# Kernel tuning notes

Measured on AMD Instinct MI355X. Metric: run time of the kernel, lower is better.

The kernel has to match this reference:

```python
import jax, jax.numpy as jnp
import numpy as np
import math

# ---- static config (matches init_kwargs) ----
LMAX = 2; NC = (LMAX + 1) ** 2        # 9 spherical components
H = 8; DQK = 32; CV = 16; K = 8       # heads, qk dim, value head dim, radial freqs
NTH = 5; NPH = 5; U = NTH * NPH       # 25 sphere directions
N = 2048; C = 256

# ---- Clebsch-Gordan in the real spherical-harmonic basis (numpy, tiny) ----
def _cg(j1, m1, j2, m2, j, m):
    if m1 + m2 != m or j < abs(j1 - j2) or j > j1 + j2:
        return 0.0
    f = math.factorial
    pref = math.sqrt((2 * j + 1) * f(j + j1 - j2) * f(j - j1 + j2) * f(j1 + j2 - j) / f(j1 + j2 + j + 1))
    pref *= math.sqrt(f(j + m) * f(j - m) * f(j1 - m1) * f(j1 + m1) * f(j2 - m2) * f(j2 + m2))
    s = 0.0
    for k in range(0, j1 + j2 - j + 1):
        d = [k, j1 + j2 - j - k, j1 - m1 - k, j2 + m2 - k, j - j2 + m1 + k, j - j1 - m2 + k]
        if min(d) < 0:
            continue
        s += (-1) ** k / (f(d[0]) * f(d[1]) * f(d[2]) * f(d[3]) * f(d[4]) * f(d[5]))
    return pref * s

def _Umat(l):
    u = np.zeros((2 * l + 1, 2 * l + 1), dtype=np.complex128)
    s = 1.0 / math.sqrt(2.0)
    for m in range(-l, l + 1):
        if m > 0:
            u[l + m, l + m] = ((-1) ** m) * s; u[l + m, l - m] = s
        elif m == 0:
            u[l, l] = 1.0
        else:
            u[l + m, l + m] = 1j * s; u[l + m, l - m] = -1j * ((-1) ** m) * s
    return u

def _real_cg(l1, l2, L):
    cgc = np.zeros((2 * l1 + 1, 2 * l2 + 1, 2 * L + 1))
    for i1, m1 in enumerate(range(-l1, l1 + 1)):
        for i2, m2 in enumerate(range(-l2, l2 + 1)):
            for i3, m3 in enumerate(range(-L, L + 1)):
                cgc[i1, i2, i3] = _cg(l1, m1, l2, m2, L, m3)
    r = np.einsum('au,bv,cw,uvw->abc', _Umat(l1), _Umat(l2), np.conj(_Umat(L)), cgc)
    re, im = np.real(r), np.imag(r)
    return re if np.linalg.norm(re) >= np.linalg.norm(im) else im

def _right_reduced():
    off = [0, 1, 4]
    R = np.zeros((NC, NC, NC)); cnt = np.zeros(LMAX + 1)
    for l1 in range(LMAX + 1):
        for l2 in range(LMAX + 1):
            for L in range(abs(l1 - l2), min(l1 + l2, LMAX) + 1):
                R[off[l1]:off[l1] + 2 * l1 + 1, off[l2]:off[l2] + 2 * l2 + 1, off[L]:off[L] + 2 * L + 1] += _real_cg(l1, l2, L)
                cnt[L] += 1
    for L in range(LMAX + 1):
        R[:, :, off[L]:off[L] + 2 * L + 1] /= max(cnt[L], 1.0)
    return R

def _sphere():
    x, w = np.polynomial.legendre.leggauss(NTH)
    phi = 2 * np.pi * np.arange(NPH) / NPH
    ct = np.repeat(x, NPH); wq = np.repeat(w, NPH) * (2 * np.pi / NPH)
    ph = np.tile(phi, NTH); st = np.sqrt(np.maximum(1 - ct * ct, 0.0))
    dirs = np.stack([st * np.cos(ph), st * np.sin(ph), ct], axis=1)
    return dirs, wq

def _ymat(d):
    x, y, z = d[:, 0], d[:, 1], d[:, 2]
    return np.stack([0.282095 * np.ones_like(x), 0.488603 * y, 0.488603 * z, 0.488603 * x,
                     1.092548 * x * y, 1.092548 * y * z, 0.315392 * (3 * z * z - 1),
                     1.092548 * x * z, 0.546274 * (x * x - y * y)], axis=0)  # [9,U]

_DIRS, _WQ = _sphere()
_YW = _ymat(_DIRS) * _WQ[None, :]          # quadrature-weighted Y_l(u): [9,U]
_RRED = _right_reduced()                    # CG coupling ell x lambda -> L<=lmax: [9,9,9]
_LDEG = np.array([0, 1, 1, 1, 2, 2, 2, 2, 2])


def setup_inputs() -> dict:
    key = jax.random.key(0)
    ks = jax.random.split(key, 8)
    node_pos = 3.0 * jax.random.normal(ks[0], (N, 3), dtype=jnp.float32)
    node_feat = jax.random.normal(ks[1], (N, NC, C), dtype=jnp.float32)
    Wq = 0.02 * jax.random.normal(ks[2], (3, C, H * DQK), dtype=jnp.float32)
    Wk = 0.02 * jax.random.normal(ks[3], (3, C, H * DQK), dtype=jnp.float32)
    Wv = jax.random.normal(ks[4], (C, H * CV), dtype=jnp.float32) / math.sqrt(C)
    Wo = jax.random.normal(ks[5], (H * CV, C), dtype=jnp.float32) / math.sqrt(H * CV)
    kappa = jnp.linspace(1.0, 1.4, K, dtype=jnp.float32)
    bias = jnp.exp(-2.0 * (kappa - 1.0) / 0.4)          # low-kappa preference at init
    a = 0.05 * jax.random.normal(ks[6], (3, H, K), dtype=jnp.float32) * bias
    return {"node_pos": node_pos, "node_feat": node_feat, "Wq": Wq, "Wk": Wk,
            "Wv": Wv, "Wo": Wo, "a": a, "kappa": kappa}


def reference(node_pos, node_feat, Wq, Wk, Wv, Wo, a, kappa):
    YW = jnp.asarray(_YW, jnp.float32)
    RRED = jnp.asarray(_RRED, jnp.float32)
    DIRS = jnp.asarray(_DIRS, jnp.float32)
    aE = a[jnp.asarray(_LDEG)]                           # [9,H,K] radial coeffs per ell component

    def so3_to_scalar(x, W):  # invariant q/k projection from irreps
        s = x[:, 0, :] @ W[0]
        s = s + jnp.sqrt(jnp.sum(x[:, 1:4, :] ** 2, axis=1) + 1e-8) @ W[1]
        s = s + jnp.sqrt(jnp.sum(x[:, 4:9, :] ** 2, axis=1) + 1e-8) @ W[2]
        return s

    q = so3_to_scalar(node_feat, Wq).reshape(-1, H, DQK)
    k = so3_to_scalar(node_feat, Wk).reshape(-1, H, DQK)
    qf = jax.nn.elu(q) + 1.0                             # linear-attention feature map
    kf = jax.nn.elu(k) + 1.0
    # value irreps per head: [N,H,Cv,lambda=9]
    v = jnp.einsum('nmc,cf->nmf', node_feat, Wv).reshape(-1, NC, H, CV).transpose(0, 2, 3, 1)

    phase = kappa[None, :, None] * (node_pos @ DIRS.T)[:, None, :]   # [N,K,U]
    cosP = jnp.cos(phase); sinP = jnp.sin(phase)

    acc = jnp.zeros((node_pos.shape[0], H, CV, NC, NC), jnp.float32)  # [N,H,Cv,lambda,ell]
    for kk in range(K):  # small fixed radial-frequency loop
        ck = cosP[:, kk]; sk = sinP[:, kk]
        Yak = jnp.einsum('eu,eh->euh', YW, aE[:, :, kk])              # a_{l,h,k} * w_u * Y_e(u)
        # moments over all nodes (keys x values x phase): [U,H,d,Cv,lambda]
        Mc = jnp.einsum('nhd,nhcl,nu->uhdcl', kf, v, ck)
        Ms = jnp.einsum('nhd,nhcl,nu->uhdcl', kf, v, sk)
        Dc = jnp.einsum('nu,euh->neuh', ck, Yak)
        Ds = jnp.einsum('nu,euh->neuh', sk, Yak)
        acc = acc + jnp.einsum('nhd,uhdcl,neuh->nhcle', qf, Mc, Dc) \
                  + jnp.einsum('nhd,uhdcl,neuh->nhcle', qf, Ms, Ds)
    Z = jnp.einsum('nhd,hd->nh', qf, kf.sum(0)) + 1e-6               # linear-attn normalizer
    acc = acc / Z[:, :, None, None, None]
    # CG coupling ell (x) lambda -> L<=lmax, path-averaged: [N,H,Cv,9]
    outm = jnp.einsum('nhcle,elm->nhcm', acc, RRED)
    out = outm.transpose(0, 3, 1, 2).reshape(-1, NC, H * CV) @ Wo    # [N,9,C]
    return out
```

## Files before the change

### kernel.cpp

```cpp
#include <hip/hip_runtime.h>
#include <cmath>
#include <complex>
#include <algorithm>


typedef _Float16 half8 __attribute__((ext_vector_type(8)));
typedef _Float16 half4v __attribute__((ext_vector_type(4)));
typedef float float4v __attribute__((ext_vector_type(4)));

namespace {

using cd = std::complex<double>;

static double fct(int n) { double r = 1.0; for (int i = 2; i <= n; ++i) r *= i; return r; }

static double cg_coef(int j1, int m1, int j2, int m2, int j, int m) {
    if (m1 + m2 != m || j < std::abs(j1 - j2) || j > j1 + j2) return 0.0;
    double pref = std::sqrt((2 * j + 1) * fct(j + j1 - j2) * fct(j - j1 + j2) * fct(j1 + j2 - j) / fct(j1 + j2 + j + 1));
    pref *= std::sqrt(fct(j + m) * fct(j - m) * fct(j1 - m1) * fct(j1 + m1) * fct(j2 - m2) * fct(j2 + m2));
    double s = 0.0;
    for (int k = 0; k <= j1 + j2 - j; ++k) {
        int d0 = k, d1 = j1 + j2 - j - k, d2 = j1 - m1 - k, d3 = j2 + m2 - k, d4 = j - j2 + m1 + k, d5 = j - j1 - m2 + k;
        if (d0 < 0 || d1 < 0 || d2 < 0 || d3 < 0 || d4 < 0 || d5 < 0) continue;
        s += ((k & 1) ? -1.0 : 1.0) / (fct(d0) * fct(d1) * fct(d2) * fct(d3) * fct(d4) * fct(d5));
    }
    return pref * s;
}

static void umat(int l, cd u[5][5]) {
    for (int i = 0; i < 5; i++) for (int j = 0; j < 5; j++) u[i][j] = cd(0, 0);
    const double s = 1.0 / std::sqrt(2.0);
    for (int m = -l; m <= l; m++) {
        double sgn = (std::abs(m) & 1) ? -1.0 : 1.0;
        if (m > 0)      { u[l + m][l + m] = cd(sgn * s, 0); u[l + m][l - m] = cd(s, 0); }
        else if (m == 0){ u[l][l] = cd(1, 0); }
        else            { u[l + m][l + m] = cd(0, s);       u[l + m][l - m] = cd(0, -sgn * s); }
    }
}

static void real_cg_f(int l1, int l2, int L, double out[5][5][5]) {
    cd U1[5][5], U2[5][5], UL[5][5];
    umat(l1, U1); umat(l2, U2); umat(L, UL);
    const int n1 = 2 * l1 + 1, n2 = 2 * l2 + 1, n3 = 2 * L + 1;
    double cgt[5][5][5];
    for (int i1 = 0; i1 < n1; i1++) for (int i2 = 0; i2 < n2; i2++) for (int i3 = 0; i3 < n3; i3++)
        cgt[i1][i2][i3] = cg_coef(l1, i1 - l1, l2, i2 - l2, L, i3 - L);
    cd r[5][5][5];
    double nr = 0, ni = 0;
    for (int a1 = 0; a1 < n1; a1++) for (int b = 0; b < n2; b++) for (int c = 0; c < n3; c++) {
        cd acc(0, 0);
        for (int uu = 0; uu < n1; uu++) for (int vv = 0; vv < n2; vv++) for (int w = 0; w < n3; w++) {
            double cval = cgt[uu][vv][w];
            if (cval == 0.0) continue;
            acc += U1[a1][uu] * U2[b][vv] * std::conj(UL[c][w]) * cval;
        }
        r[a1][b][c] = acc;
        nr += acc.real() * acc.real();
        ni += acc.imag() * acc.imag();
    }
    const bool useRe = std::sqrt(nr) >= std::sqrt(ni);
    for (int a1 = 0; a1 < n1; a1++) for (int b = 0; b < n2; b++) for (int c = 0; c < n3; c++)
        out[a1][b][c] = useRe ? r[a1][b][c].real() : r[a1][b][c].imag();
}

static float  h_const[1029];
static float* d_const_g = nullptr;

struct GlobalInit {
    GlobalInit() {
        const double PI = 3.14159265358979323846;
        const double gx[5] = {-0.9061798459386640, -0.5384693101056831, 0.0, 0.5384693101056831, 0.9061798459386640};
        const double gw[5] = { 0.23692688505618908, 0.47862867049936647, 0.5688888888888889, 0.47862867049936647, 0.23692688505618908};
        double YW[9][25], DIRS[25][3];
        for (int u = 0; u < 25; ++u) {
            const int it = u / 5, ip = u % 5;
            const double ct = gx[it], wq = gw[it] * (2.0 * PI / 5.0), ph = 2.0 * PI * ip / 5.0;
            const double st = std::sqrt(std::max(1.0 - ct * ct, 0.0));
            const double x = st * std::cos(ph), y = st * std::sin(ph), z = ct;
            DIRS[u][0] = x; DIRS[u][1] = y; DIRS[u][2] = z;
            double Y[9];
            Y[0] = 0.282095;           Y[1] = 0.488603 * y;      Y[2] = 0.488603 * z;
            Y[3] = 0.488603 * x;       Y[4] = 1.092548 * x * y;  Y[5] = 1.092548 * y * z;
            Y[6] = 0.315392 * (3 * z * z - 1); Y[7] = 1.092548 * x * z; Y[8] = 0.546274 * (x * x - y * y);
            for (int e = 0; e < 9; e++) YW[e][u] = Y[e] * wq;
        }
        double RRED[9][9][9];
        for (int i = 0; i < 9; i++) for (int j = 0; j < 9; j++) for (int k = 0; k < 9; k++) RRED[i][j][k] = 0.0;
        const int off[3] = {0, 1, 4};
        double cnt[3] = {0, 0, 0};
        double rc[5][5][5];
        for (int l1 = 0; l1 <= 2; l1++) for (int l2 = 0; l2 <= 2; l2++) {
            const int Llo = std::abs(l1 - l2), Lhi = std::min(l1 + l2, 2);
            for (int L = Llo; L <= Lhi; L++) {
                real_cg_f(l1, l2, L, rc);
                for (int i1 = 0; i1 < 2 * l1 + 1; i1++)
                    for (int i2 = 0; i2 < 2 * l2 + 1; i2++)
                        for (int i3 = 0; i3 < 2 * L + 1; i3++)
                            RRED[off[l1] + i1][off[l2] + i2][off[L] + i3] += rc[i1][i2][i3];
                cnt[L] += 1.0;
            }
        }
        for (int L = 0; L <= 2; L++) {
            const double dv = std::max(cnt[L], 1.0);
            for (int a1 = 0; a1 < 9; a1++) for (int b = 0; b < 9; b++)
                for (int k = 0; k < 2 * L + 1; k++) RRED[a1][b][off[L] + k] /= dv;
        }
        for (int e = 0; e < 9; e++) for (int u = 0; u < 25; u++) h_const[e * 25 + u] = (float)YW[e][u];
        for (int e = 0; e < 9; e++) for (int l = 0; l < 9; l++) for (int m = 0; m < 9; m++)
            h_const[225 + e * 81 + l * 9 + m] = (float)RRED[e][l][m];
        for (int u = 0; u < 25; u++) for (int ax = 0; ax < 3; ax++) h_const[954 + u * 3 + ax] = (float)DIRS[u][ax];
        if (hipMalloc((void**)&d_const_g, 1029 * sizeof(float)) == hipSuccess)
            hipMemcpy(d_const_g, h_const, 1029 * sizeof(float), hipMemcpyHostToDevice);
    }
} g_init;

}


__global__ void radial_k(const float* __restrict__ feat, float* __restrict__ R) {
    const int n = blockIdx.x, c = threadIdx.x;
    const float* f = feat + (size_t)n * 9 * 256 + c;
    const float f0 = f[0];
    const float a1 = f[256], a2 = f[512], a3 = f[768];
    const float b1 = f[1024], b2 = f[1280], b3 = f[1536], b4 = f[1792], b5 = f[2048];
    const float r1 = sqrtf(a1 * a1 + a2 * a2 + a3 * a3 + 1e-8f);
    const float r2 = sqrtf(b1 * b1 + b2 * b2 + b3 * b3 + b4 * b4 + b5 * b5 + 1e-8f);
    float* o = R + (size_t)n * 768 + c;
    o[0] = f0; o[256] = r1; o[512] = r2;
}

__global__ __launch_bounds__(256) void qk_gemm_k(const float* __restrict__ A,
                                                 const float* __restrict__ Wq,
                                                 const float* __restrict__ Wk,
                                                 float* __restrict__ qf,
                                                 _Float16* __restrict__ kfA) {
    __shared__ __align__(16) _Float16 Af[64 * 40];
    __shared__ __align__(16) _Float16 Bf[64 * 40];
    const int tid = threadIdx.x;
    const int w = tid >> 6, lane = tid & 63;
    const int l15 = lane & 15, quad = lane >> 4;
    const bool isK = blockIdx.x >= 4;
    const int cb = (blockIdx.x & 3) * 64;
    const int rb = blockIdx.y * 64;
    const float* B = isK ? Wk : Wq;
    const int N = 256, Kd = 768;
    const int sr = tid >> 2, sq = tid & 3;

    float4v acc[4];
#pragma unroll
    for (int s = 0; s < 4; s++) acc[s] = float4v{0.f, 0.f, 0.f, 0.f};

    for (int k0 = 0; k0 < Kd; k0 += 32) {
        __syncthreads();
        {
            const float* Ap = A + (size_t)(rb + sr) * Kd + k0 + sq * 8;
            const float4 a0 = *(const float4*)(Ap);
            const float4 a1 = *(const float4*)(Ap + 4);
            half8 hv;
            hv[0] = (_Float16)a0.x; hv[1] = (_Float16)a0.y; hv[2] = (_Float16)a0.z; hv[3] = (_Float16)a0.w;
            hv[4] = (_Float16)a1.x; hv[5] = (_Float16)a1.y; hv[6] = (_Float16)a1.z; hv[7] = (_Float16)a1.w;
            *(half8*)&Af[sr * 40 + sq * 8] = hv;
        }
        {
            const float* Bp = B + (size_t)(k0 + sq * 8) * N + cb + sr;
            half8 hv;
#pragma unroll
            for (int i = 0; i < 8; i++) hv[i] = (_Float16)Bp[(size_t)i * N];
            *(half8*)&Bf[sr * 40 + sq * 8] = hv;
        }
        __syncthreads();
        const half8 af = *(const half8*)&Af[(w * 16 + l15) * 40 + quad * 8];
#pragma unroll
        for (int s = 0; s < 4; s++) {
            const half8 bf = *(const half8*)&Bf[(s * 16 + l15) * 40 + quad * 8];
            acc[s] = __builtin_amdgcn_mfma_f32_16x16x32_f16(af, bf, acc[s], 0, 0, 0);
        }
    }
#pragma unroll
    for (int s = 0; s < 4; s++) {
#pragma unroll
        for (int r = 0; r < 4; r++) {
            const int row = rb + w * 16 + quad * 4 + r;
            const int col = cb + s * 16 + l15;
            float val = acc[s][r];
            val = (val > 0.f ? val : expf(val) - 1.f) + 1.f;
            if (isK) {
                const int hh = col >> 5, dd = col & 31, tt = dd >> 4, ll = dd & 15;
                kfA[(size_t)hh * 65536 + (size_t)(row >> 5) * 1024 + tt * 512 + ll * 32 + (row & 31)] = (_Float16)val;
            } else {
                qf[(size_t)row * 256 + col] = val;
            }
        }
    }
}

__global__ __launch_bounds__(256) void mfma_gemm16_k(const float* __restrict__ A, const float* __restrict__ B,
                                                     float* __restrict__ Cv, int M, int N, int Kd, int mode,
                                                     const float* __restrict__ rZ) {
    __shared__ __align__(16) _Float16 Af[64 * 40];
    __shared__ __align__(16) _Float16 Bf[64 * 40];
    const int tid = threadIdx.x;
    const int w = tid >> 6, lane = tid & 63;
    const int l15 = lane & 15, quad = lane >> 4;
    const int rb = blockIdx.y * 64, cb = blockIdx.x * 64;
    const int sr = tid >> 2, sq = tid & 3;

    float4v acc[4];
#pragma unroll
    for (int s = 0; s < 4; s++) acc[s] = float4v{0.f, 0.f, 0.f, 0.f};

    for (int k0 = 0; k0 < Kd; k0 += 32) {
        __syncthreads();
        if (mode == 4) {
            const _Float16* Ap16 = (const _Float16*)A + (size_t)(rb + sr) * Kd + k0 + sq * 8;
            const half8 p0 = *(const half8*)(Ap16);
            const half8 p1 = *(const half8*)(Ap16 + 2359296);
            const half8 p2 = *(const half8*)(Ap16 + 4718592);
            const half8 p3 = *(const half8*)(Ap16 + 7077888);
            const int n = (rb + sr) / 9;
            const int hh = (k0 + sq * 8) >> 4;
            const float rz = rZ[n * 8 + hh];
            half8 hv;
#pragma unroll
            for (int i = 0; i < 8; i++)
                hv[i] = (_Float16)(((float)p0[i] + (float)p1[i] + (float)p2[i] + (float)p3[i]) * rz);
            *(half8*)&Af[sr * 40 + sq * 8] = hv;
        } else {
            const float* Ap = A + (size_t)(rb + sr) * Kd + k0 + sq * 8;
            const float4 a0 = *(const float4*)(Ap);
            const float4 a1 = *(const float4*)(Ap + 4);
            half8 hv;
            hv[0] = (_Float16)a0.x; hv[1] = (_Float16)a0.y; hv[2] = (_Float16)a0.z; hv[3] = (_Float16)a0.w;
            hv[4] = (_Float16)a1.x; hv[5] = (_Float16)a1.y; hv[6] = (_Float16)a1.z; hv[7] = (_Float16)a1.w;
            *(half8*)&Af[sr * 40 + sq * 8] = hv;
        }
        {
            const float* Bp = B + (size_t)(k0 + sq * 8) * N + cb + sr;
            half8 hv;
#pragma unroll
            for (int i = 0; i < 8; i++) hv[i] = (_Float16)Bp[(size_t)i * N];
            *(half8*)&Bf[sr * 40 + sq * 8] = hv;
        }
        __syncthreads();
        const half8 af = *(const half8*)&Af[(w * 16 + l15) * 40 + quad * 8];
#pragma unroll
        for (int s = 0; s < 4; s++) {
            const half8 bf = *(const half8*)&Bf[(s * 16 + l15) * 40 + quad * 8];
            acc[s] = __builtin_amdgcn_mfma_f32_16x16x32_f16(af, bf, acc[s], 0, 0, 0);
        }
    }
#pragma unroll
    for (int s = 0; s < 4; s++) {
#pragma unroll
        for (int r = 0; r < 4; r++) {
            const int row = rb + w * 16 + quad * 4 + r;
            const int col = cb + s * 16 + l15;
            float val = acc[s][r];
            if (mode == 2) {
                const int n = row / 9, l = row - n * 9, hq = col >> 4, cvq = col & 15;
                _Float16* o = (_Float16*)Cv;
                o[((size_t)hq * 144 + cvq * 9 + l) * 2048 + n] = (_Float16)val;
            } else {
                Cv[(size_t)row * N + col] = val;
            }
        }
    }
}

__global__ void trig_k(const float* __restrict__ pos, const float* __restrict__ kappa,
                       const float* __restrict__ cst, _Float16* __restrict__ trigA) {
    const int n = blockIdx.x, t = threadIdx.x;
    const size_t base = (size_t)(n >> 5) * 16384 + (n & 31);
    if (t < 200) {
        const int kq = t / 25, u = t - kq * 25;
        const float* dirs = cst + 954;
        const float ph = kappa[kq] * (pos[n * 3] * dirs[u * 3] + pos[n * 3 + 1] * dirs[u * 3 + 1] + pos[n * 3 + 2] * dirs[u * 3 + 2]);
        float s, c;
        sincosf(ph, &s, &c);
        const int kkut = (kq * 25 + u) * 2;
        trigA[base + (size_t)kkut * 32] = (_Float16)c;
        trigA[base + (size_t)(kkut + 1) * 32] = (_Float16)s;
    } else {
        const int kkut = 400 + (t - 200) * 2;
        trigA[base + (size_t)kkut * 32] = (_Float16)0.f;
        trigA[base + (size_t)(kkut + 1) * 32] = (_Float16)0.f;
    }
}

__global__ void ksumT_k(const _Float16* __restrict__ kfA, float* __restrict__ ksum) {
    const int b = blockIdx.x;
    const int h = b >> 5, d = b & 31, t = d >> 4, l15 = d & 15;
    const int i = threadIdx.x;
    const half8 v = *(const half8*)(kfA + (size_t)h * 65536 + (size_t)(i >> 2) * 1024 + t * 512 + l15 * 32 + (i & 3) * 8);
    float s = 0.f;
#pragma unroll
    for (int k = 0; k < 8; k++) s += (float)v[k];
#pragma unroll
    for (int off = 32; off > 0; off >>= 1) s += __shfl_down(s, off, 64);
    __shared__ float red[4];
    if ((i & 63) == 0) red[i >> 6] = s;
    __syncthreads();
    if (i == 0) ksum[b] = red[0] + red[1] + red[2] + red[3];
}

__global__ void zg_k(const float* __restrict__ qf, const float* __restrict__ ksum, float* __restrict__ rz,
                     const float* __restrict__ a, const float* __restrict__ cst, float* __restrict__ G) {
    if (blockIdx.x < 64) {
        const int idx = blockIdx.x * 256 + threadIdx.x;
        const int n = idx >> 3, h = idx & 7;
        float s = 0.f;
#pragma unroll
        for (int d = 0; d < 32; d++) s += qf[(size_t)n * 256 + h * 32 + d] * ksum[h * 32 + d];
        rz[idx] = 1.0f / (s + 1e-6f);
    } else {
        const int b = blockIdx.x - 64;
        const int kk = b & 7, h = b >> 3;
        __shared__ float ae[9];
        if (threadIdx.x < 9) {
            const int ldeg[9] = {0, 1, 1, 1, 2, 2, 2, 2, 2};
            ae[threadIdx.x] = a[ldeg[threadIdx.x] * 64 + h * 8 + kk];
        }
        __syncthreads();
        const float* yw = cst;
        const float* rred = cst + 225;
        for (int i = threadIdx.x; i < 25 * 81; i += 256) {
            const int u = i / 81, lm = i - u * 81;
            float s = 0.f;
#pragma unroll
            for (int e = 0; e < 9; e++) s += ae[e] * yw[e * 25 + u] * rred[e * 81 + lm];
            G[((size_t)(kk * 8 + h) * 25 + u) * 81 + lm] = s;
        }
    }
}

__global__ __launch_bounds__(256, 3) void multipole_mm_k(const _Float16* __restrict__ trigA,
                                                         const _Float16* __restrict__ kfA,
                                                         const _Float16* __restrict__ v16T,
                                                         _Float16* __restrict__ M16) {
    const int h   = blockIdx.x;
    const int tid = threadIdx.x;
    const int w = tid >> 6, lane = tid & 63;
    const int l15 = lane & 15, quad = lane >> 4;
    const int cb  = blockIdx.y * 512 + w * 128;
    const int cl0 = cb >> 5;
    const int r0  = blockIdx.z * 32;

    __shared__ __align__(16) _Float16 sb[2][20][512];

    float4v acc[2][8];
#pragma unroll
    for (int rt = 0; rt < 2; rt++)
#pragma unroll
        for (int s = 0; s < 8; s++) acc[rt][s] = float4v{0.f, 0.f, 0.f, 0.f};

    const _Float16* afg0 = trigA + (size_t)(r0 + l15) * 32 + quad * 8;
    const _Float16* afg1 = afg0 + 512;
    const _Float16* kqg0 = kfA + (size_t)h * 65536 + (size_t)l15 * 32 + quad * 8;
    const _Float16* kqg1 = kqg0 + 512;
    const int vs = lane >> 4, vc = (lane >> 2) & 3, vg = lane & 3;
    const _Float16* vqg = v16T + (size_t)(h * 144 + cl0 + vc) * 2048 + vs * 32 + vg * 8;

    half8 g0, g1, g2, g3, g4;

#define GATHER(nbr_) { \
        const size_t t5 = (size_t)((nbr_) >> 5) + w; \
        g0 = *(const half8*)(afg0 + t5 * 16384); \
        g1 = *(const half8*)(afg1 + t5 * 16384); \
        g2 = *(const half8*)(kqg0 + t5 * 1024); \
        g3 = *(const half8*)(kqg1 + t5 * 1024); \
        g4 = *(const half8*)(vqg + (nbr_)); }

#define DSWRITE(b_) { \
        *(half8*)&sb[b_][w * 4 + 0][lane * 8] = g0; \
        *(half8*)&sb[b_][w * 4 + 1][lane * 8] = g1; \
        *(half8*)&sb[b_][w * 4 + 2][lane * 8] = g2; \
        *(half8*)&sb[b_][w * 4 + 3][lane * 8] = g3; \
        *(half8*)&sb[b_][16 + w][lane * 8] = g4; }

#define STEP(s_) { \
        const half8 af0 = *(const half8*)&sb[cur][(s_) * 4 + 0][lane * 8]; \
        const half8 af1 = *(const half8*)&sb[cur][(s_) * 4 + 1][lane * 8]; \
        const half8 kq0 = *(const half8*)&sb[cur][(s_) * 4 + 2][lane * 8]; \
        const half8 kq1 = *(const half8*)&sb[cur][(s_) * 4 + 3][lane * 8]; \
        _Pragma("unroll") \
        for (int c = 0; c < 4; c++) { \
            const half8 vq = *(const half8*)&sb[cur][16 + w][((s_) * 4 + c) * 32 + quad * 8]; \
            const half8 b0 = kq0 * vq; \
            const half8 b1 = kq1 * vq; \
            acc[0][2 * c]     = __builtin_amdgcn_mfma_f32_16x16x32_f16(af0, b0, acc[0][2 * c],     0, 0, 0); \
            acc[0][2 * c + 1] = __builtin_amdgcn_mfma_f32_16x16x32_f16(af0, b1, acc[0][2 * c + 1], 0, 0, 0); \
            acc[1][2 * c]     = __builtin_amdgcn_mfma_f32_16x16x32_f16(af1, b0, acc[1][2 * c],     0, 0, 0); \
            acc[1][2 * c + 1] = __builtin_amdgcn_mfma_f32_16x16x32_f16(af1, b1, acc[1][2 * c + 1], 0, 0, 0); \
        } }

    int cur = 0;
    GATHER(0)
    DSWRITE(0)
    __syncthreads();
#pragma unroll 1
    for (int r = 0; r < 16; ++r) {
        if (r < 15) GATHER((r + 1) * 128)
        STEP(0)
        STEP(1)
        STEP(2)
        STEP(3)
        if (r < 15) DSWRITE(cur ^ 1)
        __syncthreads();
        cur ^= 1;
    }

#undef GATHER
#undef DSWRITE
#undef STEP

#pragma unroll
    for (int rt = 0; rt < 2; rt++)
#pragma unroll
        for (int c = 0; c < 4; c++)
#pragma unroll
            for (int half = 0; half < 2; half++)
#pragma unroll
                for (int r = 0; r < 4; r++) {
                    const int row = r0 + rt * 16 + quad * 4 + r;
                    const int col = cb + c * 32 + half * 16 + l15;
                    M16[((size_t)row * 8 + h) * 4608 + col] = (_Float16)acc[rt][c * 2 + half][r];
                }
}

__global__ __launch_bounds__(256) void fold_k(const _Float16* __restrict__ Mv, const float* __restrict__ G,
                                              _Float16* __restrict__ MG) {
    const int kt = blockIdx.x, h = blockIdx.y;
    const int tid = threadIdx.x;
    __shared__ float ms[144 * 33];
    __shared__ float gs[81];
    const _Float16* src = Mv + ((size_t)kt * 8 + h) * 4608;
    for (int i = tid; i < 4608; i += 256) {
        const int cl = i >> 5, d = i & 31;
        ms[cl * 33 + d] = (float)src[i];
    }
    const int kk = kt / 50, u = (kt >> 1) % 25;
    if (tid < 81) gs[tid] = G[(((size_t)kk * 8 + h) * 25 + u) * 81 + tid];
    __syncthreads();
    _Float16* dst = MG + ((size_t)kt * 8 + h) * 4608;
    for (int i = tid; i < 4608; i += 256) {
        const int ct = i >> 9, quad = (i >> 7) & 3, l15 = (i >> 3) & 15, j = i & 7;
        const int d = quad * 8 + j;
        const int cm = ct * 16 + l15, c = cm / 9, m = cm - c * 9;
        float s = 0.f;
#pragma unroll
        for (int l = 0; l < 9; l++) s += ms[(c * 9 + l) * 33 + d] * gs[l * 9 + m];
        dst[i] = (_Float16)s;
    }
}

__global__ __launch_bounds__(256, 1) void mm_local_k(const float* __restrict__ qf, const _Float16* __restrict__ trigA,
                                                     const _Float16* __restrict__ MG, _Float16* __restrict__ outp) {
    const int combo = blockIdx.y * 8 + blockIdx.x;
    const int h = combo >> 2;
    const int slice = combo & 3;
    const int n0 = blockIdx.z * 256;
    const int tid = threadIdx.x;
    const int w = tid >> 6, lane = tid & 63;
    const int l15 = lane & 15, quad = lane >> 4;

    __shared__ __align__(16) _Float16 sb[2][4][4608];

    const int nbase = n0 + w * 64;
    half8 qfr16[4];
#pragma unroll
    for (int rt = 0; rt < 4; rt++) {
        const int n = nbase + rt * 16 + l15;
        const float* qp = qf + (size_t)n * 256 + h * 32 + quad * 8;
#pragma unroll
        for (int j = 0; j < 8; j++) qfr16[rt][j] = (_Float16)qp[j];
    }
    float4v acc[4][9];
#pragma unroll
    for (int rt = 0; rt < 4; rt++)
#pragma unroll
        for (int ct = 0; ct < 9; ct++) acc[rt][ct] = float4v{0.f, 0.f, 0.f, 0.f};

    const int kt0 = slice * 100;
    const _Float16* mg0 = MG + (((size_t)kt0 * 8 + h) * 4608) + lane * 8;
    const _Float16* trg0 = trigA + (size_t)(nbase >> 5) * 16384 + (size_t)kt0 * 32 + l15;

#define STAGE(b_, r_) { \
        const _Float16* src = mg0 + (size_t)((r_) * 4 + w) * 8 * 4608; \
        _Float16* dstl = &sb[b_][w][0]; \
        _Pragma("unroll") \
        for (int i = 0; i < 9; i++) \
            __builtin_amdgcn_global_load_lds( \
                (const __attribute__((address_space(1))) void*)(src + i * 512), \
                (__attribute__((address_space(3))) void*)(dstl + i * 512), 16, 0, 0); }

    _Float16 ta[4], tb[4], tc[4], td[4], ua[4], ub[4], uc[4], ud[4];
    int cur = 0;
    STAGE(0, 0)
#pragma unroll
    for (int kl = 0; kl < 4; kl++) {
        ta[kl] = trg0[kl * 32];           tb[kl] = trg0[kl * 32 + 16];
        tc[kl] = trg0[16384 + kl * 32];   td[kl] = trg0[16384 + kl * 32 + 16];
    }
    __syncthreads();

#pragma unroll 1
    for (int r = 0; r < 25; ++r) {
        if (r < 24) {
            STAGE(cur ^ 1, r + 1)
#pragma unroll
            for (int kl = 0; kl < 4; kl++) {
                const size_t o = (size_t)((r + 1) * 4 + kl) * 32;
                ua[kl] = trg0[o];           ub[kl] = trg0[o + 16];
                uc[kl] = trg0[16384 + o];   ud[kl] = trg0[16384 + o + 16];
            }
        }
#pragma unroll
        for (int kl = 0; kl < 4; kl++) {
            half8 tv0, tv1, tv2, tv3;
#pragma unroll
            for (int j = 0; j < 8; j++) { tv0[j] = ta[kl]; tv1[j] = tb[kl]; tv2[j] = tc[kl]; tv3[j] = td[kl]; }
            const half8 af0 = tv0 * qfr16[0];
            const half8 af1 = tv1 * qfr16[1];
            const half8 af2 = tv2 * qfr16[2];
            const half8 af3 = tv3 * qfr16[3];
#pragma unroll
            for (int ct = 0; ct < 9; ct++) {
                const half8 b = *(const half8*)&sb[cur][kl][ct * 512 + quad * 128 + l15 * 8];
                acc[0][ct] = __builtin_amdgcn_mfma_f32_16x16x32_f16(af0, b, acc[0][ct], 0, 0, 0);
                acc[1][ct] = __builtin_amdgcn_mfma_f32_16x16x32_f16(af1, b, acc[1][ct], 0, 0, 0);
                acc[2][ct] = __builtin_amdgcn_mfma_f32_16x16x32_f16(af2, b, acc[2][ct], 0, 0, 0);
                acc[3][ct] = __builtin_amdgcn_mfma_f32_16x16x32_f16(af3, b, acc[3][ct], 0, 0, 0);
            }
        }
        __syncthreads();
        cur ^= 1;
#pragma unroll
        for (int kl = 0; kl < 4; kl++) { ta[kl] = ua[kl]; tb[kl] = ub[kl]; tc[kl] = uc[kl]; td[kl] = ud[kl]; }
    }
#undef STAGE

    float* ebp = (float*)sb;
    _Float16* dst = outp + (size_t)slice * 2359296;
    const int g4 = lane >> 2, sub = lane & 3;
#pragma unroll
    for (int rt = 0; rt < 4; rt++) {
        __syncthreads();
#pragma unroll
        for (int ct = 0; ct < 9; ct++) {
            const int cm = ct * 16 + l15;
            const int c = cm / 9, m = cm - c * 9;
#pragma unroll
            for (int r = 0; r < 4; r++)
                ebp[(size_t)(w * 16 + quad * 4 + r) * 148 + m * 16 + c] = acc[rt][ct][r];
        }
        __syncthreads();
#pragma unroll
        for (int s = 0; s < 9; s++) {
            const int li = s * 16 + g4;
            const int nl = li / 9, m = li - nl * 9;
            const float4 v4 = *(const float4*)&ebp[(size_t)(w * 16 + nl) * 148 + m * 16 + sub * 4];
            const int n = nbase + rt * 16 + nl;
            half4v hv;
            hv[0] = (_Float16)v4.x; hv[1] = (_Float16)v4.y; hv[2] = (_Float16)v4.z; hv[3] = (_Float16)v4.w;
            *(half4v*)&dst[((size_t)n * 9 + m) * 128 + h * 16 + sub * 4] = hv;
        }
    }
}

extern "C" void kernel_launch(void* const* d_in, const int* in_sizes, int n_in,
                              void* d_out, int out_size, void* d_ws, size_t ws_size,
                              hipStream_t stream) {
    const float* pos  = (const float*)d_in[0];
    const float* feat = (const float*)d_in[1];
    const float* Wq   = (const float*)d_in[2];
    const float* Wk   = (const float*)d_in[3];
    const float* Wv   = (const float*)d_in[4];
    const float* Wo   = (const float*)d_in[5];
    const float* a    = (const float*)d_in[6];
    const float* kap  = (const float*)d_in[7];
    float* out = (float*)d_out;
    float* ws = (float*)d_ws;

    float* qf    = ws;
    float* kfAF  = qf + 524288;
    float* vTF   = kfAF + 262144;
    float* trigF = vTF + 1179648;
    float* ksum  = trigF + 524288;
    float* rz    = ksum + 256;
    float* G     = rz + 16384;
    float* M16F  = G + 129600;
    float* regX  = M16F + 9437184;
    float* R     = regX;
    _Float16* trigA = (_Float16*)trigF;
    _Float16* kfA   = (_Float16*)kfAF;
    _Float16* v16T  = (_Float16*)vTF;
    _Float16* M16   = (_Float16*)M16F;
    _Float16* MG16  = (_Float16*)regX;
    _Float16* outp16 = (_Float16*)M16F;

    const float* cst = d_const_g;

    hipLaunchKernelGGL(radial_k, dim3(2048), dim3(256), 0, stream, feat, R);
    hipLaunchKernelGGL(qk_gemm_k, dim3(8, 32), dim3(256), 0, stream, R, Wq, Wk, qf, kfA);
    hipLaunchKernelGGL(mfma_gemm16_k, dim3(2, 288), dim3(256), 0, stream, feat, Wv, vTF, 18432, 128, 256, 2, rz);
    hipLaunchKernelGGL(trig_k, dim3(2048), dim3(256), 0, stream, pos, kap, cst, trigA);
    hipLaunchKernelGGL(ksumT_k, dim3(256), dim3(256), 0, stream, kfA, ksum);
    hipLaunchKernelGGL(zg_k, dim3(128), dim3(256), 0, stream, qf, ksum, rz, a, cst, G);
    hipLaunchKernelGGL(multipole_mm_k, dim3(8, 9, 13), dim3(256), 0, stream, trigA, kfA, v16T, M16);
    hipLaunchKernelGGL(fold_k, dim3(400, 8), dim3(256), 0, stream, M16, G, MG16);
    hipLaunchKernelGGL(mm_local_k, dim3(8, 4, 8), dim3(256), 0, stream, qf, trigA, MG16, outp16);
    hipLaunchKernelGGL(mfma_gemm16_k, dim3(4, 288), dim3(256), 0, stream, (const float*)outp16, Wo, out, 18432, 256, 128, 4, rz);
}
```

Before: 320.1 us.

## Split mm_local reduction into eight slices and fold slice-sum into output GEMM

The local multipole kernel now splits its 200 k-steps across 8 slices instead of 4. That doubles the block count, and launch bounds allow two blocks per CU to improve latency hiding; the odd tail of steps is handled with a half stage. The 1/Z normalisation moves into the mm_local epilogue. The final Wo GEMM treats the slice partials as a K=1024 reduction instead of summing four partials while loading. In exchange, twice as much partial-output data is written and read, and the workspace must hold eight slices.

```diff
diff --git a/kernel.cpp b/kernel.cpp
--- a/kernel.cpp
+++ b/kernel.cpp
@@ -212,19 +212,10 @@
     for (int k0 = 0; k0 < Kd; k0 += 32) {
         __syncthreads();
         if (mode == 4) {
-            const _Float16* Ap16 = (const _Float16*)A + (size_t)(rb + sr) * Kd + k0 + sq * 8;
-            const half8 p0 = *(const half8*)(Ap16);
-            const half8 p1 = *(const half8*)(Ap16 + 2359296);
-            const half8 p2 = *(const half8*)(Ap16 + 4718592);
-            const half8 p3 = *(const half8*)(Ap16 + 7077888);
-            const int n = (rb + sr) / 9;
-            const int hh = (k0 + sq * 8) >> 4;
-            const float rz = rZ[n * 8 + hh];
-            half8 hv;
-#pragma unroll
-            for (int i = 0; i < 8; i++)
-                hv[i] = (_Float16)(((float)p0[i] + (float)p1[i] + (float)p2[i] + (float)p3[i]) * rz);
-            *(half8*)&Af[sr * 40 + sq * 8] = hv;
+            const int s8 = k0 >> 7;
+            const int j0 = (k0 & 127) + sq * 8;
+            const _Float16* Ap16 = (const _Float16*)A + (size_t)s8 * 2359296 + (size_t)(rb + sr) * 128 + j0;
+            *(half8*)&Af[sr * 40 + sq * 8] = *(const half8*)Ap16;
         } else {
             const float* Ap = A + (size_t)(rb + sr) * Kd + k0 + sq * 8;
             const float4 a0 = *(const float4*)(Ap);
@@ -235,7 +226,8 @@
             *(half8*)&Af[sr * 40 + sq * 8] = hv;
         }
         {
-            const float* Bp = B + (size_t)(k0 + sq * 8) * N + cb + sr;
+            const int brow = (mode == 4) ? ((k0 & 127) + sq * 8) : (k0 + sq * 8);
+            const float* Bp = B + (size_t)brow * N + cb + sr;
             half8 hv;
 #pragma unroll
             for (int i = 0; i < 8; i++) hv[i] = (_Float16)Bp[(size_t)i * N];
@@ -453,17 +445,19 @@
     }
 }
 
-__global__ __launch_bounds__(256, 1) void mm_local_k(const float* __restrict__ qf, const _Float16* __restrict__ trigA,
-                                                     const _Float16* __restrict__ MG, _Float16* __restrict__ outp) {
+__global__ __launch_bounds__(256, 2) void mm_local_k(const float* __restrict__ qf, const _Float16* __restrict__ trigA,
+                                                     const _Float16* __restrict__ MG, const float* __restrict__ rZ,
+                                                     _Float16* __restrict__ outp) {
     const int combo = blockIdx.y * 8 + blockIdx.x;
-    const int h = combo >> 2;
-    const int slice = combo & 3;
+    const int h = combo >> 3;
+    const int slice = combo & 7;
     const int n0 = blockIdx.z * 256;
     const int tid = threadIdx.x;
     const int w = tid >> 6, lane = tid & 63;
     const int l15 = lane & 15, quad = lane >> 4;
 
-    __shared__ __align__(16) _Float16 sb[2][4][4608];
+    __shared__ __align__(16) unsigned char smem_raw[73728];
+    _Float16 (*sb)[4][4608] = (_Float16 (*)[4][4608])smem_raw;
 
     const int nbase = n0 + w * 64;
     half8 qfr16[4];
@@ -480,22 +474,40 @@
 #pragma unroll
         for (int ct = 0; ct < 9; ct++) acc[rt][ct] = float4v{0.f, 0.f, 0.f, 0.f};
 
-    const int kt0 = slice * 100;
+    const int kt0 = slice * 50;
     const _Float16* mg0 = MG + (((size_t)kt0 * 8 + h) * 4608) + lane * 8;
     const _Float16* trg0 = trigA + (size_t)(nbase >> 5) * 16384 + (size_t)kt0 * 32 + l15;
 
-#define STAGE(b_, r_) { \
-        const _Float16* src = mg0 + (size_t)((r_) * 4 + w) * 8 * 4608; \
+#define STAGE4(b_, base_) { \
+        const _Float16* src = mg0 + (size_t)((base_) + w) * 8 * 4608; \
         _Float16* dstl = &sb[b_][w][0]; \
         _Pragma("unroll") \
         for (int i = 0; i < 9; i++) \
             __builtin_amdgcn_global_load_lds( \
                 (const __attribute__((address_space(1))) void*)(src + i * 512), \
                 (__attribute__((address_space(3))) void*)(dstl + i * 512), 16, 0, 0); }
+#define STAGE2(b_, base_) if (w < 2) STAGE4(b_, base_)
+
+#define COMPUTE(kl) { \
+        half8 tv0, tv1, tv2, tv3; \
+        _Pragma("unroll") \
+        for (int j = 0; j < 8; j++) { tv0[j] = ta[kl]; tv1[j] = tb[kl]; tv2[j] = tc[kl]; tv3[j] = td[kl]; } \
+        const half8 af0 = tv0 * qfr16[0]; \
+        const half8 af1 = tv1 * qfr16[1]; \
+        const half8 af2 = tv2 * qfr16[2]; \
+        const half8 af3 = tv3 * qfr16[3]; \
+        _Pragma("unroll") \
+        for (int ct = 0; ct < 9; ct++) { \
+            const half8 b = *(const half8*)&sb[cur][kl][ct * 512 + quad * 128 + l15 * 8]; \
+            acc[0][ct] = __builtin_amdgcn_mfma_f32_16x16x32_f16(af0, b, acc[0][ct], 0, 0, 0); \
+            acc[1][ct] = __builtin_amdgcn_mfma_f32_16x16x32_f16(af1, b, acc[1][ct], 0, 0, 0); \
+            acc[2][ct] = __builtin_amdgcn_mfma_f32_16x16x32_f16(af2, b, acc[2][ct], 0, 0, 0); \
+            acc[3][ct] = __builtin_amdgcn_mfma_f32_16x16x32_f16(af3, b, acc[3][ct], 0, 0, 0); \
+        } }
 
     _Float16 ta[4], tb[4], tc[4], td[4], ua[4], ub[4], uc[4], ud[4];
     int cur = 0;
-    STAGE(0, 0)
+    STAGE4(0, 0)
 #pragma unroll
     for (int kl = 0; kl < 4; kl++) {
         ta[kl] = trg0[kl * 32];           tb[kl] = trg0[kl * 32 + 16];
@@ -504,42 +516,39 @@
     __syncthreads();
 
 #pragma unroll 1
-    for (int r = 0; r < 25; ++r) {
-        if (r < 24) {
-            STAGE(cur ^ 1, r + 1)
+    for (int r = 0; r < 12; ++r) {
+        if (r < 11) {
+            STAGE4(cur ^ 1, (r + 1) * 4)
 #pragma unroll
             for (int kl = 0; kl < 4; kl++) {
                 const size_t o = (size_t)((r + 1) * 4 + kl) * 32;
                 ua[kl] = trg0[o];           ub[kl] = trg0[o + 16];
                 uc[kl] = trg0[16384 + o];   ud[kl] = trg0[16384 + o + 16];
             }
-        }
-#pragma unroll
-        for (int kl = 0; kl < 4; kl++) {
-            half8 tv0, tv1, tv2, tv3;
-#pragma unroll
-            for (int j = 0; j < 8; j++) { tv0[j] = ta[kl]; tv1[j] = tb[kl]; tv2[j] = tc[kl]; tv3[j] = td[kl]; }
-            const half8 af0 = tv0 * qfr16[0];
-            const half8 af1 = tv1 * qfr16[1];
-            const half8 af2 = tv2 * qfr16[2];
-            const half8 af3 = tv3 * qfr16[3];
-#pragma unroll
-            for (int ct = 0; ct < 9; ct++) {
-                const half8 b = *(const half8*)&sb[cur][kl][ct * 512 + quad * 128 + l15 * 8];
-                acc[0][ct] = __builtin_amdgcn_mfma_f32_16x16x32_f16(af0, b, acc[0][ct], 0, 0, 0);
-                acc[1][ct] = __builtin_amdgcn_mfma_f32_16x16x32_f16(af1, b, acc[1][ct], 0, 0, 0);
-                acc[2][ct] = __builtin_amdgcn_mfma_f32_16x16x32_f16(af2, b, acc[2][ct], 0, 0, 0);
-                acc[3][ct] = __builtin_amdgcn_mfma_f32_16x16x32_f16(af3, b, acc[3][ct], 0, 0, 0);
+        } else {
+            STAGE2(cur ^ 1, 48)
+#pragma unroll
+            for (int kl = 0; kl < 2; kl++) {
+                const size_t o = (size_t)(48 + kl) * 32;
+                ua[kl] = trg0[o];           ub[kl] = trg0[o + 16];
+                uc[kl] = trg0[16384 + o];   ud[kl] = trg0[16384 + o + 16];
             }
-        }
+            ua[2] = ub[2] = uc[2] = ud[2] = (_Float16)0.f;
+            ua[3] = ub[3] = uc[3] = ud[3] = (_Float16)0.f;
+        }
+        COMPUTE(0) COMPUTE(1) COMPUTE(2) COMPUTE(3)
         __syncthreads();
         cur ^= 1;
 #pragma unroll
         for (int kl = 0; kl < 4; kl++) { ta[kl] = ua[kl]; tb[kl] = ub[kl]; tc[kl] = uc[kl]; td[kl] = ud[kl]; }
     }
-#undef STAGE
-
-    float* ebp = (float*)sb;
+    COMPUTE(0) COMPUTE(1)
+
+#undef STAGE4
+#undef STAGE2
+#undef COMPUTE
+
+    float* ebp = (float*)smem_raw;
     _Float16* dst = outp + (size_t)slice * 2359296;
     const int g4 = lane >> 2, sub = lane & 3;
 #pragma unroll
@@ -560,8 +569,10 @@
             const int nl = li / 9, m = li - nl * 9;
             const float4 v4 = *(const float4*)&ebp[(size_t)(w * 16 + nl) * 148 + m * 16 + sub * 4];
             const int n = nbase + rt * 16 + nl;
+            const float rzv = rZ[(size_t)n * 8 + h];
             half4v hv;
-            hv[0] = (_Float16)v4.x; hv[1] = (_Float16)v4.y; hv[2] = (_Float16)v4.z; hv[3] = (_Float16)v4.w;
+            hv[0] = (_Float16)(v4.x * rzv); hv[1] = (_Float16)(v4.y * rzv);
+            hv[2] = (_Float16)(v4.z * rzv); hv[3] = (_Float16)(v4.w * rzv);
             *(half4v*)&dst[((size_t)n * 9 + m) * 128 + h * 16 + sub * 4] = hv;
         }
     }
@@ -608,6 +619,6 @@
     hipLaunchKernelGGL(zg_k, dim3(128), dim3(256), 0, stream, qf, ksum, rz, a, cst, G);
     hipLaunchKernelGGL(multipole_mm_k, dim3(8, 9, 13), dim3(256), 0, stream, trigA, kfA, v16T, M16);
     hipLaunchKernelGGL(fold_k, dim3(400, 8), dim3(256), 0, stream, M16, G, MG16);
-    hipLaunchKernelGGL(mm_local_k, dim3(8, 4, 8), dim3(256), 0, stream, qf, trigA, MG16, outp16);
-    hipLaunchKernelGGL(mfma_gemm16_k, dim3(4, 288), dim3(256), 0, stream, (const float*)outp16, Wo, out, 18432, 256, 128, 4, rz);
-}
+    hipLaunchKernelGGL(mm_local_k, dim3(8, 8, 8), dim3(256), 0, stream, qf, trigA, MG16, rz, outp16);
+    hipLaunchKernelGGL(mfma_gemm16_k, dim3(4, 288), dim3(256), 0, stream, (const float*)outp16, Wo, out, 18432, 256, 1024, 4, rz);
+}
```

Measured after the change: 345.3 us. +7.9%, slower.
